# Optimization experiments

Hardware: AMD Instinct MI355X
Metric: run time of the kernel (lower is better)

The kernel has to match this reference:

```python
import jax, jax.numpy as jnp
import numpy as np
from jax import lax

B, M, N = 4096, 306, 984
LAMBDA = 0.1
MAX_ITER = 50


def setup_inputs() -> dict:
    key = jax.random.key(0)
    k1, k2, k3, k4 = jax.random.split(key, 4)
    return {
        "r_real": jax.random.normal(k1, (B, M), dtype=jnp.float32),
        "r_imag": jax.random.normal(k2, (B, M), dtype=jnp.float32),
        # phi buffer: torch.randn(M, N, dtype=complex64) -> real/imag each ~N(0, 1/2)?
        # torch.randn(complex64) draws real & imag each from N(0, 1/sqrt(2)^2)=N(0,0.5).
        "phi_real": jax.random.normal(k3, (M, N), dtype=jnp.float32) * np.float32(1.0 / np.sqrt(2.0)),
        "phi_imag": jax.random.normal(k4, (M, N), dtype=jnp.float32) * np.float32(1.0 / np.sqrt(2.0)),
    }


def reference(r_real, r_imag, phi_real, phi_imag):
    phi = (phi_real + 1j * phi_imag).astype(jnp.complex64)          # [M, N]
    r = (r_real + 1j * r_imag).astype(jnp.complex64)                # [B, M]
    # step_size = 1 / ||phi||_2^2  (spectral norm squared)
    step = (1.0 / jnp.linalg.norm(phi, ord=2) ** 2).real.astype(jnp.float32)
    thresh = (LAMBDA * step).astype(jnp.float32)
    phi_c = jnp.conj(phi)

    def body(w, _):
        # error = w @ phi.T - r : [B, M]
        error = jnp.einsum("bn,mn->bm", w, phi) - r
        # gradient = error @ conj(phi) : [B, N]
        grad = jnp.einsum("bm,mn->bn", error, phi_c)
        w_next = w - step * grad
        w_mag = jnp.abs(w_next)
        new_mag = jax.nn.relu(w_mag - thresh)
        # polar(new_mag, angle(w_next))
        w_new = (new_mag * jnp.exp(1j * jnp.angle(w_next))).astype(jnp.complex64)
        return w_new, None

    w0 = jnp.zeros((r.shape[0], N), dtype=jnp.complex64)
    w, _ = lax.scan(body, w0, None, length=MAX_ITER)
    return jnp.abs(w).astype(jnp.float32)
```

## Files before the change

kernel.cpp:

```cpp
#include <hip/hip_runtime.h>
#include <math.h>

#define Bb 4096
#define Mm 306
#define Nn 984
#define NCP 1024
#define KA 2048
#define ITERS 50
#define KSQ 9

typedef _Float16 f16x8 __attribute__((ext_vector_type(8)));
typedef float f32x16 __attribute__((ext_vector_type(16)));

__device__ __forceinline__ void cmac(float2& c, const float2 a, const float2 b) {
    c.x = fmaf(a.x, b.x, c.x);
    c.x = fmaf(-a.y, b.y, c.x);
    c.y = fmaf(a.x, b.y, c.y);
    c.y = fmaf(a.y, b.x, c.y);
}

__device__ __forceinline__ unsigned short f16bits(float v) {
    union { _Float16 h; unsigned short u; } cv;
    cv.h = (_Float16)v;
    return cv.u;
}
__device__ __forceinline__ float f16lo(unsigned int u) {
    union { unsigned short s; _Float16 h; } cv; cv.s = (unsigned short)(u & 0xffffu);
    return (float)cv.h;
}
__device__ __forceinline__ float f16hi(unsigned int u) {
    union { unsigned short s; _Float16 h; } cv; cv.s = (unsigned short)(u >> 16);
    return (float)cv.h;
}

__device__ __forceinline__ void load_lds16(const void* g, void* l) {
    __builtin_amdgcn_global_load_lds((const __attribute__((address_space(1))) void*)g,
                                     (__attribute__((address_space(3))) void*)l, 16, 0, 0);
}

__device__ __forceinline__ size_t swzA(int b, int c) {
    return ((size_t)(((b >> 7) * 32 + (c >> 5)) * 1024 + ((c >> 2) & 7) * 128 + (b & 127))) * 4 + (c & 3);
}
__device__ __forceinline__ size_t swzB(int jr, int q) {
    return ((size_t)(((jr >> 7) * 32 + (q >> 5)) * 1024 + ((q >> 2) & 7) * 128 + (jr & 127))) * 4 + (q & 3);
}
__device__ __forceinline__ size_t swzA2(int b, int c) {
    return ((size_t)(((b >> 7) * 10 + (c >> 5)) * 1024 + ((c >> 2) & 7) * 128 + (b & 127))) * 4 + (c & 3);
}
__device__ __forceinline__ size_t swzB2(int jr, int q) {
    return ((size_t)(((jr >> 7) * 10 + (q >> 5)) * 1024 + ((q >> 2) & 7) * 128 + (jr & 127))) * 4 + (q & 3);
}

__global__ void gram_kernel(const float* __restrict__ pr, const float* __restrict__ pi,
                            float2* __restrict__ G) {
    __shared__ float2 As[32][33];
    __shared__ float2 Bs[32][33];
    int tx = threadIdx.x, ty = threadIdx.y;
    int t = ty * 16 + tx;
    int i0 = blockIdx.y * 32, j0 = blockIdx.x * 32;
    int zs = blockIdx.z * 246;
    int ze = zs + 246 < Nn ? zs + 246 : Nn;
    float2 acc[2][2] = {};
    for (int k0 = zs; k0 < ze; k0 += 32) {
        #pragma unroll
        for (int rep = 0; rep < 4; ++rep) {
            int idx = t + rep * 256;
            int rr = idx >> 5, cc = idx & 31;
            int gk = k0 + cc;
            int gi = i0 + rr, gj = j0 + rr;
            float2 a = make_float2(0.f, 0.f), b = make_float2(0.f, 0.f);
            if (gk < ze) {
                if (gi < Mm) a = make_float2(pr[(size_t)gi * Nn + gk], pi[(size_t)gi * Nn + gk]);
                if (gj < Mm) b = make_float2(pr[(size_t)gj * Nn + gk], pi[(size_t)gj * Nn + gk]);
            }
            As[rr][cc] = a; Bs[rr][cc] = b;
        }
        __syncthreads();
        #pragma unroll 8
        for (int kk = 0; kk < 32; ++kk) {
            float2 a0 = As[ty * 2][kk], a1 = As[ty * 2 + 1][kk];
            float2 b0 = Bs[tx * 2][kk], b1 = Bs[tx * 2 + 1][kk];
            #define GMAC(qq, aa, bb) \
                qq.x = fmaf(aa.x, bb.x, qq.x); qq.x = fmaf(aa.y, bb.y, qq.x); \
                qq.y = fmaf(aa.y, bb.x, qq.y); qq.y = fmaf(-aa.x, bb.y, qq.y);
            GMAC(acc[0][0], a0, b0) GMAC(acc[0][1], a0, b1)
            GMAC(acc[1][0], a1, b0) GMAC(acc[1][1], a1, b1)
            #undef GMAC
        }
        __syncthreads();
    }
    #pragma unroll
    for (int i = 0; i < 2; ++i) {
        int gi = i0 + ty * 2 + i;
        #pragma unroll
        for (int j = 0; j < 2; ++j) {
            int gj = j0 + tx * 2 + j;
            if (gi < Mm && gj < Mm) {
                atomicAdd(&G[gi * Mm + gj].x, acc[i][j].x);
                atomicAdd(&G[gi * Mm + gj].y, acc[i][j].y);
            }
        }
    }
}

__global__ void frobz_kernel(const float2* __restrict__ H, float* __restrict__ slot,
                             float2* __restrict__ dst, int n) {
    int idx = blockIdx.x * blockDim.x + threadIdx.x;
    int stride = gridDim.x * blockDim.x;
    float s = 0.f;
    for (int i = idx; i < n; i += stride) {
        float2 v = H[i];
        s = fmaf(v.x, v.x, s);
        s = fmaf(v.y, v.y, s);
        dst[i] = make_float2(0.f, 0.f);
    }
    #pragma unroll
    for (int o = 32; o > 0; o >>= 1) s += __shfl_down(s, o, 64);
    __shared__ float wsum[4];
    int lane = threadIdx.x & 63, wv = threadIdx.x >> 6;
    if (lane == 0) wsum[wv] = s;
    __syncthreads();
    if (threadIdx.x == 0) atomicAdd(slot, wsum[0] + wsum[1] + wsum[2] + wsum[3]);
}

__global__ void sqmm_kernel(const float2* __restrict__ A, float2* __restrict__ C,
                            const float* __restrict__ fslot) {
    __shared__ float2 As[32][33];
    __shared__ float2 Bs[32][33];
    float inv = 1.0f / fslot[0];
    int tx = threadIdx.x, ty = threadIdx.y;
    int t = ty * 16 + tx;
    int r0 = blockIdx.y * 32, c0 = blockIdx.x * 32;
    int zs = blockIdx.z * 80;
    int ze = zs + 80 < Mm ? zs + 80 : Mm;
    float2 acc[2][2] = {};
    for (int k0 = zs; k0 < ze; k0 += 32) {
        #pragma unroll
        for (int i = 0; i < 4; ++i) {
            int idx = t + i * 256;
            int rr = idx >> 5, cc = idx & 31;
            int gr = r0 + rr, gk = k0 + cc;
            As[rr][cc] = (gr < Mm && gk < ze) ? A[gr * Mm + gk] : make_float2(0.f, 0.f);
            int gk2 = k0 + rr, gc = c0 + cc;
            Bs[rr][cc] = (gk2 < ze && gc < Mm) ? A[gk2 * Mm + gc] : make_float2(0.f, 0.f);
        }
        __syncthreads();
        #pragma unroll 8
        for (int kk = 0; kk < 32; ++kk) {
            float2 a0 = As[ty * 2][kk], a1 = As[ty * 2 + 1][kk];
            float2 b0 = Bs[kk][tx * 2], b1 = Bs[kk][tx * 2 + 1];
            cmac(acc[0][0], a0, b0); cmac(acc[0][1], a0, b1);
            cmac(acc[1][0], a1, b0); cmac(acc[1][1], a1, b1);
        }
        __syncthreads();
    }
    #pragma unroll
    for (int i = 0; i < 2; ++i) {
        int gr = r0 + ty * 2 + i;
        #pragma unroll
        for (int j = 0; j < 2; ++j) {
            int gc = c0 + tx * 2 + j;
            if (gr < Mm && gc < Mm) {
                atomicAdd(&C[gr * Mm + gc].x, acc[i][j].x * inv);
                atomicAdd(&C[gr * Mm + gc].y, acc[i][j].y * inv);
            }
        }
    }
}

__global__ void ray1_kernel(const float2* __restrict__ H, float2* __restrict__ v) {
    int t = blockIdx.x;
    int k = threadIdx.x;
    float sx = 0.f, sy = 0.f;
    for (int j = k; j < Mm; j += 256) {
        float2 h = H[(size_t)t * Mm + j];
        sx += h.x; sy += h.y;
    }
    #pragma unroll
    for (int o = 32; o > 0; o >>= 1) { sx += __shfl_down(sx, o, 64); sy += __shfl_down(sy, o, 64); }
    __shared__ float wx[4], wy[4];
    int lane = k & 63, wv = k >> 6;
    if (lane == 0) { wx[wv] = sx; wy[wv] = sy; }
    __syncthreads();
    if (k == 0) v[t] = make_float2(wx[0] + wx[1] + wx[2] + wx[3],
                                   wy[0] + wy[1] + wy[2] + wy[3]);
}

__global__ void ray2_kernel(const float2* __restrict__ G, const float2* __restrict__ v,
                            float* __restrict__ slots) {
    int t = blockIdx.x;
    int k0 = threadIdx.x;
    float ux = 0.f, uy = 0.f;
    for (int k = k0; k < Mm; k += 256) {
        float2 g = G[(size_t)k * Mm + t];
        float2 vk = v[k];
        ux = fmaf(g.x, vk.x, ux); ux = fmaf(g.y, vk.y, ux);
        uy = fmaf(g.x, vk.y, uy); uy = fmaf(-g.y, vk.x, uy);
    }
    #pragma unroll
    for (int o = 32; o > 0; o >>= 1) { ux += __shfl_down(ux, o, 64); uy += __shfl_down(uy, o, 64); }
    __shared__ float wx[4], wy[4];
    int lane = k0 & 63, wv = k0 >> 6;
    if (lane == 0) { wx[wv] = ux; wy[wv] = uy; }
    __syncthreads();
    if (k0 == 0) {
        float sux = wx[0] + wx[1] + wx[2] + wx[3];
        float suy = wy[0] + wy[1] + wy[2] + wy[3];
        float2 vt = v[t];
        atomicAdd(&slots[16], vt.x * sux + vt.y * suy);
        atomicAdd(&slots[17], vt.x * vt.x + vt.y * vt.y);
    }
}

__global__ void ray3_kernel(const float* __restrict__ slots, float* __restrict__ sc) {
    float step = slots[17] / slots[16];
    sc[0] = step;
    sc[1] = 0.1f * step;
}

__global__ void qpack_kernel(const float* __restrict__ pr, const float* __restrict__ pi,
                             unsigned int* __restrict__ Bu, const float* __restrict__ sc) {
    __shared__ float2 Pn[16][33];
    __shared__ float2 Pc[16][65];
    float nstep = -sc[0];
    int t = threadIdx.x;
    int tx = t & 15, ty = t >> 4;
    int n0 = blockIdx.x * 32, c0 = blockIdx.y * 64;
    float2 q[2][4] = {};
    for (int m0 = 0; m0 < Mm; m0 += 16) {
        #pragma unroll
        for (int rep = 0; rep < 6; ++rep) {
            int idx = t + rep * 256;
            if (idx < 512) {
                int mm = idx >> 5, col = idx & 31;
                int gm = m0 + mm;
                float2 a = make_float2(0.f, 0.f);
                if (gm < Mm && n0 + col < Nn)
                    a = make_float2(pr[(size_t)gm * Nn + n0 + col], pi[(size_t)gm * Nn + n0 + col]);
                Pn[mm][col] = a;
            } else {
                int idx2 = idx - 512;
                int mm = idx2 >> 6, col = idx2 & 63;
                int gm = m0 + mm;
                float2 b = make_float2(0.f, 0.f);
                if (gm < Mm && c0 + col < Nn)
                    b = make_float2(pr[(size_t)gm * Nn + c0 + col], pi[(size_t)gm * Nn + c0 + col]);
                Pc[mm][col] = b;
            }
        }
        __syncthreads();
        #pragma unroll
        for (int mm = 0; mm < 16; ++mm) {
            float2 a0 = Pn[mm][ty * 2], a1 = Pn[mm][ty * 2 + 1];
            float2 b0 = Pc[mm][tx * 4], b1 = Pc[mm][tx * 4 + 1];
            float2 b2 = Pc[mm][tx * 4 + 2], b3 = Pc[mm][tx * 4 + 3];
            #define QMAC(qq, aa, bb) \
                qq.x = fmaf(aa.x, bb.x, qq.x); qq.x = fmaf(aa.y, bb.y, qq.x); \
                qq.y = fmaf(aa.y, bb.x, qq.y); qq.y = fmaf(-aa.x, bb.y, qq.y);
            QMAC(q[0][0], a0, b0) QMAC(q[0][1], a0, b1) QMAC(q[0][2], a0, b2) QMAC(q[0][3], a0, b3)
            QMAC(q[1][0], a1, b0) QMAC(q[1][1], a1, b1) QMAC(q[1][2], a1, b2) QMAC(q[1][3], a1, b3)
            #undef QMAC
        }
        __syncthreads();
    }
    #pragma unroll
    for (int i = 0; i < 2; ++i) {
        int n = n0 + ty * 2 + i;
        #pragma unroll
        for (int j = 0; j < 4; ++j) {
            int c = c0 + tx * 4 + j;
            if (n < Nn && c < Nn) {
                float MR = fmaf(nstep, q[i][j].x, (n == c) ? 1.0f : 0.0f);
                float MI = nstep * q[i][j].y;
                unsigned short hR = f16bits(MR);
                unsigned short hI = f16bits(MI);
                unsigned short nhI = hI ^ 0x8000u;
                int jr = ((c >> 5) * 64) + (c & 31);
                Bu[swzB(jr, n)]      = (unsigned)hR | ((unsigned)nhI << 16);
                Bu[swzB(jr + 32, n)] = (unsigned)hI | ((unsigned)hR << 16);
            }
        }
    }
}

__global__ void rpack_kernel(const float* __restrict__ rr, const float* __restrict__ ri,
                             unsigned int* __restrict__ rp16) {
    int b = blockIdx.x * 256 + threadIdx.x;
    int m = blockIdx.y;
    rp16[swzA2(b, m)] = (unsigned)f16bits(rr[(size_t)b * Mm + m]) |
                        ((unsigned)f16bits(ri[(size_t)b * Mm + m]) << 16);
}

__global__ void ppack2_kernel(const float* __restrict__ pr, const float* __restrict__ pi,
                              unsigned int* __restrict__ B2u, const float* __restrict__ sc) {
    int n = blockIdx.x * 256 + threadIdx.x;
    int m = blockIdx.y;
    if (n >= Nn) return;
    float s = sc[0];
    float xr = pr[(size_t)m * Nn + n], xi = pi[(size_t)m * Nn + n];
    unsigned short x = f16bits(-s * xr), y = f16bits(-s * xi);
    int jr2 = ((n >> 5) * 64) + (n & 31);
    B2u[swzB2(jr2, m)]      = (unsigned)x | ((unsigned)y << 16);
    B2u[swzB2(jr2 + 32, m)] = (unsigned)(y ^ 0x8000u) | ((unsigned)x << 16);
}

__global__ __launch_bounds__(256, 2) void rphi_mfma_kernel(
    const _Float16* __restrict__ rp16, const _Float16* __restrict__ B2,
    unsigned int* __restrict__ rph16) {
    __shared__ _Float16 As[8192];
    __shared__ _Float16 Bs[8192];
    int tid = threadIdx.x;
    int lane = tid & 63, wv = tid >> 6;
    int wm = wv & 1, wn = wv >> 1;
    int bblk = blockIdx.x, nblk = blockIdx.y;
    int l31 = lane & 31, lh = lane >> 5;

    f32x16 acc[2][2] = {};

    for (int kt = 0; kt < 10; ++kt) {
        #pragma unroll
        for (int c = 0; c < 4; ++c) {
            int u = c * 256 + tid;
            const char* ga = (const char*)rp16 + (((size_t)(bblk * 10 + kt)) * 1024 + u) * 16;
            load_lds16(ga, &As[(size_t)(c * 256 + wv * 64) * 8]);
            const char* gb = (const char*)B2 + (((size_t)(nblk * 10 + kt)) * 1024 + u) * 16;
            load_lds16(gb, &Bs[(size_t)(c * 256 + wv * 64) * 8]);
        }
        __syncthreads();
        #pragma unroll
        for (int s = 0; s < 4; ++s) {
            int kq = s * 2 + lh;
            f16x8 af[2], bfr[2];
            #pragma unroll
            for (int mt = 0; mt < 2; ++mt)
                af[mt] = *reinterpret_cast<const f16x8*>(
                    &As[(size_t)(kq * 128 + wm * 64 + mt * 32 + l31) * 8]);
            #pragma unroll
            for (int nt = 0; nt < 2; ++nt)
                bfr[nt] = *reinterpret_cast<const f16x8*>(
                    &Bs[(size_t)(kq * 128 + wn * 64 + nt * 32 + l31) * 8]);
            #pragma unroll
            for (int mt = 0; mt < 2; ++mt)
                #pragma unroll
                for (int nt = 0; nt < 2; ++nt)
                    acc[mt][nt] = __builtin_amdgcn_mfma_f32_32x32x16_f16(af[mt], bfr[nt], acc[mt][nt], 0, 0, 0);
        }
        __syncthreads();
    }

    int b0 = bblk * 128;
    int c = nblk * 64 + wn * 32 + l31;
    #pragma unroll
    for (int mt = 0; mt < 2; ++mt) {
        #pragma unroll
        for (int reg = 0; reg < 16; ++reg) {
            int row = b0 + wm * 64 + mt * 32 + ((reg & 3) + 8 * (reg >> 2) + 4 * lh);
            rph16[(size_t)row * NCP + c] =
                (unsigned)f16bits(-acc[mt][0][reg]) | ((unsigned)f16bits(-acc[mt][1][reg]) << 16);
        }
    }
}

__global__ __launch_bounds__(512) void ista9_kernel(
    const _Float16* __restrict__ wfi, const _Float16* __restrict__ Bq,
    unsigned int* __restrict__ wfo,
    const unsigned int* __restrict__ rph16,
    const float* __restrict__ sc, float* __restrict__ out, int last) {
    __shared__ _Float16 As0[8192], As1[8192];
    __shared__ _Float16 Bs0[2][8192], Bs1[2][8192];
    int tid = threadIdx.x;
    int lane = tid & 63, wv = tid >> 6;
    int wm = wv >> 2, wn = wv & 3;
    int id = blockIdx.x;
    int x = id & 7;
    int n = id >> 3;
    int bblk = (x & 3) * 8 + (n & 7);
    int nb2  = (x >> 2) * 4 + (n >> 3);
    int l31 = lane & 31, lh = lane >> 5;
    int slab = wn >> 1, chg = wn & 1;

    f32x16 acc[2][2] = {};

    const char* gA  = (const char*)wfi + (size_t)bblk * 32 * 1024 * 16;
    const char* gB0 = (const char*)Bq + (size_t)(nb2 * 2 + 0) * 32 * 1024 * 16;
    const char* gB1 = (const char*)Bq + (size_t)(nb2 * 2 + 1) * 32 * 1024 * 16;

    #define STAGE9(kt, Ad, Bd)                                                        \
        {                                                                             \
            _Float16* Ap = (Ad);                                                      \
            _Float16* Bp0 = &(Bd)[0][0];                                              \
            _Float16* Bp1 = &(Bd)[1][0];                                              \
            _Pragma("unroll")                                                         \
            for (int cc = 0; cc < 2; ++cc) {                                          \
                int u = cc * 512 + tid;                                               \
                size_t ldst = (size_t)(cc * 512 + wv * 64) * 8;                       \
                load_lds16(gA + ((size_t)(kt) * 1024 + u) * 16, &Ap[ldst]);           \
                load_lds16(gB0 + ((size_t)(kt) * 1024 + u) * 16, &Bp0[ldst]);         \
                load_lds16(gB1 + ((size_t)(kt) * 1024 + u) * 16, &Bp1[ldst]);         \
            }                                                                         \
        }

    #define COMPUTE9(Asrc, Bsrc)                                                      \
        {                                                                             \
            _Pragma("unroll")                                                         \
            for (int s = 0; s < 4; ++s) {                                             \
                int kq = s * 2 + lh;                                                  \
                f16x8 af[2], bf[2];                                                   \
                _Pragma("unroll")                                                     \
                for (int mt = 0; mt < 2; ++mt)                                        \
                    af[mt] = *reinterpret_cast<const f16x8*>(                         \
                        &(Asrc)[(size_t)(kq * 128 + wm * 64 + mt * 32 + l31) * 8]);   \
                _Pragma("unroll")                                                     \
                for (int nt = 0; nt < 2; ++nt)                                        \
                    bf[nt] = *reinterpret_cast<const f16x8*>(                         \
                        &(Bsrc)[slab][(size_t)(kq * 128 + chg * 64 + nt * 32 + l31) * 8]); \
                _Pragma("unroll")                                                     \
                for (int mt = 0; mt < 2; ++mt)                                        \
                    _Pragma("unroll")                                                 \
                    for (int nt = 0; nt < 2; ++nt)                                    \
                        acc[mt][nt] = __builtin_amdgcn_mfma_f32_32x32x16_f16(         \
                            af[mt], bf[nt], acc[mt][nt], 0, 0, 0);                    \
            }                                                                         \
        }

    STAGE9(0, As0, Bs0);
    for (int kt = 0; kt < 32; kt += 2) {
        STAGE9(kt + 1, As1, Bs1);
        asm volatile("s_waitcnt vmcnt(6)" ::: "memory");
        __builtin_amdgcn_s_barrier();
        COMPUTE9(As0, Bs0);
        __builtin_amdgcn_s_barrier();
        STAGE9(kt + 2, As0, Bs0);
        asm volatile("s_waitcnt vmcnt(6)" ::: "memory");
        __builtin_amdgcn_s_barrier();
        COMPUTE9(As1, Bs1);
        __builtin_amdgcn_s_barrier();
    }
    #undef STAGE9
    #undef COMPUTE9

    float thr = sc[1];
    int b0 = bblk * 128;
    int c = nb2 * 128 + wn * 32 + l31;
    #pragma unroll
    for (int mt = 0; mt < 2; ++mt) {
        #pragma unroll
        for (int reg = 0; reg < 16; ++reg) {
            int row = b0 + wm * 64 + mt * 32 + ((reg & 3) + 8 * (reg >> 2) + 4 * lh);
            unsigned int ru = rph16[(size_t)row * NCP + c];
            float zr = acc[mt][0][reg] + f16lo(ru);
            float zi = acc[mt][1][reg] + f16hi(ru);
            float mag = sqrtf(zr * zr + zi * zi);
            float nm = mag - thr;
            float f = (nm > 0.f) ? (nm / mag) : 0.f;
            wfo[swzA(row, c)] = (unsigned)f16bits(zr * f) | ((unsigned)f16bits(zi * f) << 16);
            if (last && c < Nn) out[(size_t)row * Nn + c] = fmaxf(nm, 0.f);
        }
    }
}

extern "C" void kernel_launch(void* const* d_in, const int* in_sizes, int n_in,
                              void* d_out, int out_size, void* d_ws, size_t ws_size,
                              hipStream_t stream) {
    const float* rr = (const float*)d_in[0];
    const float* ri = (const float*)d_in[1];
    const float* pr = (const float*)d_in[2];
    const float* pi = (const float*)d_in[3];
    float* out = (float*)d_out;

    char* ws = (char*)d_ws;
    size_t off = 0;
    _Float16* wf0 = (_Float16*)(ws + off); off += (size_t)Bb * KA * sizeof(_Float16);
    _Float16* wf1 = (_Float16*)(ws + off); off += (size_t)Bb * KA * sizeof(_Float16);
    _Float16* Bq  = (_Float16*)(ws + off); off += (size_t)2048 * 2048 * sizeof(_Float16);
    unsigned int* rph16 = (unsigned int*)(ws + off); off += (size_t)Bb * NCP * 4;
    _Float16* rp16 = (_Float16*)(ws + off); off += (size_t)Bb * 640 * sizeof(_Float16);
    _Float16* B2  = (_Float16*)(ws + off); off += (size_t)2048 * 640 * sizeof(_Float16);
    float2* G = (float2*)(ws + off);     off += (size_t)Mm * Mm * sizeof(float2);
    float2* H1 = (float2*)(ws + off);    off += (size_t)Mm * Mm * sizeof(float2);
    float2* H2 = (float2*)(ws + off);    off += (size_t)Mm * Mm * sizeof(float2);
    float2* vvec = (float2*)(ws + off);  off += (size_t)Mm * sizeof(float2);
    float* slots = (float*)(ws + off);   off += 64 * sizeof(float);
    float* sc = slots + 32;

    (void)hipMemsetAsync(wf0, 0, (size_t)Bb * KA * sizeof(_Float16), stream);
    (void)hipMemsetAsync(Bq, 0, (size_t)2048 * 2048 * sizeof(_Float16), stream);
    (void)hipMemsetAsync(rp16, 0, (size_t)Bb * 640 * sizeof(_Float16), stream);
    (void)hipMemsetAsync(B2, 0, (size_t)2048 * 640 * sizeof(_Float16), stream);
    (void)hipMemsetAsync(slots, 0, 64 * sizeof(float), stream);
    (void)hipMemsetAsync(G, 0, (size_t)Mm * Mm * sizeof(float2), stream);

    gram_kernel<<<dim3(10, 10, 4), dim3(16, 16), 0, stream>>>(pr, pi, G);
    float2* bufs[2] = { H1, H2 };
    const float2* src = G;
    for (int s = 0; s < KSQ; ++s) {
        float2* dst = bufs[s & 1];
        frobz_kernel<<<128, 256, 0, stream>>>(src, slots + s, dst, Mm * Mm);
        sqmm_kernel<<<dim3(10, 10, 4), dim3(16, 16), 0, stream>>>(src, dst, slots + s);
        src = dst;
    }
    ray1_kernel<<<Mm, 256, 0, stream>>>(src, vvec);
    ray2_kernel<<<Mm, 256, 0, stream>>>(G, vvec, slots);
    ray3_kernel<<<1, 1, 0, stream>>>(slots, sc);

    qpack_kernel<<<dim3(31, 16), 256, 0, stream>>>(pr, pi, (unsigned int*)Bq, sc);
    rpack_kernel<<<dim3(16, Mm), 256, 0, stream>>>(rr, ri, (unsigned int*)rp16);
    ppack2_kernel<<<dim3(4, Mm), 256, 0, stream>>>(pr, pi, (unsigned int*)B2, sc);
    rphi_mfma_kernel<<<dim3(32, 16), 256, 0, stream>>>(rp16, B2, rph16);

    _Float16* wbuf[2] = { wf0, wf1 };
    for (int it = 0; it < ITERS; ++it) {
        ista9_kernel<<<256, 512, 0, stream>>>(
            wbuf[it & 1], Bq, (unsigned int*)wbuf[(it + 1) & 1], rph16, sc, out,
            it == ITERS - 1 ? 1 : 0);
    }
}
```

Measured before the change: 2.882 ms.

## Interleave ISTA MFMA phases with split global-to-LDS staging and priority hints

The ISTA iteration kernel's k-tile compute is split into four barrier-separated phases. Part of the next tile's B prefetch is issued inside the first phase, and each MFMA group is wrapped in s_setprio so waves overlap memory issue with matrix math. The vmcnt wait drops from 6 to 4 to match the new load split. The one-time qpack kernel also changes its column mapping to strided per-thread access, meant to reduce LDS bank conflicts. The cost is many more workgroup barriers per tile, which may add stalls.

```diff
diff --git a/kernel.cpp b/kernel.cpp
--- a/kernel.cpp
+++ b/kernel.cpp
@@ -252,8 +252,8 @@
         #pragma unroll
         for (int mm = 0; mm < 16; ++mm) {
             float2 a0 = Pn[mm][ty * 2], a1 = Pn[mm][ty * 2 + 1];
-            float2 b0 = Pc[mm][tx * 4], b1 = Pc[mm][tx * 4 + 1];
-            float2 b2 = Pc[mm][tx * 4 + 2], b3 = Pc[mm][tx * 4 + 3];
+            float2 b0 = Pc[mm][tx], b1 = Pc[mm][16 + tx];
+            float2 b2 = Pc[mm][32 + tx], b3 = Pc[mm][48 + tx];
             #define QMAC(qq, aa, bb) \
                 qq.x = fmaf(aa.x, bb.x, qq.x); qq.x = fmaf(aa.y, bb.y, qq.x); \
                 qq.y = fmaf(aa.y, bb.x, qq.y); qq.y = fmaf(-aa.x, bb.y, qq.y);
@@ -268,7 +268,7 @@
         int n = n0 + ty * 2 + i;
         #pragma unroll
         for (int j = 0; j < 4; ++j) {
-            int c = c0 + tx * 4 + j;
+            int c = c0 + j * 16 + tx;
             if (n < Nn && c < Nn) {
                 float MR = fmaf(nstep, q[i][j].x, (n == c) ? 1.0f : 0.0f);
                 float MI = nstep * q[i][j].y;
@@ -361,7 +361,7 @@
     }
 }
 
-__global__ __launch_bounds__(512) void ista9_kernel(
+__global__ __launch_bounds__(512) void ista10_kernel(
     const _Float16* __restrict__ wfi, const _Float16* __restrict__ Bq,
     unsigned int* __restrict__ wfo,
     const unsigned int* __restrict__ rph16,
@@ -385,59 +385,65 @@
     const char* gB0 = (const char*)Bq + (size_t)(nb2 * 2 + 0) * 32 * 1024 * 16;
     const char* gB1 = (const char*)Bq + (size_t)(nb2 * 2 + 1) * 32 * 1024 * 16;
 
-    #define STAGE9(kt, Ad, Bd)                                                        \
+    #define STAGE_A(kt, Ad, Bd)                                                       \
         {                                                                             \
-            _Float16* Ap = (Ad);                                                      \
-            _Float16* Bp0 = &(Bd)[0][0];                                              \
-            _Float16* Bp1 = &(Bd)[1][0];                                              \
-            _Pragma("unroll")                                                         \
-            for (int cc = 0; cc < 2; ++cc) {                                          \
-                int u = cc * 512 + tid;                                               \
-                size_t ldst = (size_t)(cc * 512 + wv * 64) * 8;                       \
-                load_lds16(gA + ((size_t)(kt) * 1024 + u) * 16, &Ap[ldst]);           \
-                load_lds16(gB0 + ((size_t)(kt) * 1024 + u) * 16, &Bp0[ldst]);         \
-                load_lds16(gB1 + ((size_t)(kt) * 1024 + u) * 16, &Bp1[ldst]);         \
-            }                                                                         \
-        }
-
-    #define COMPUTE9(Asrc, Bsrc)                                                      \
+            size_t ld0 = (size_t)(wv * 64) * 8;                                       \
+            size_t ld1 = (size_t)(512 + wv * 64) * 8;                                 \
+            load_lds16(gA + ((size_t)(kt) * 1024 + tid) * 16, &(Ad)[ld0]);            \
+            load_lds16(gB0 + ((size_t)(kt) * 1024 + tid) * 16, &(Bd)[0][ld0]);        \
+            load_lds16(gB1 + ((size_t)(kt) * 1024 + tid) * 16, &(Bd)[1][ld0]);        \
+            load_lds16(gA + ((size_t)(kt) * 1024 + 512 + tid) * 16, &(Ad)[ld1]);      \
+        }
+    #define STAGE_B(kt, Bd)                                                           \
         {                                                                             \
-            _Pragma("unroll")                                                         \
-            for (int s = 0; s < 4; ++s) {                                             \
-                int kq = s * 2 + lh;                                                  \
-                f16x8 af[2], bf[2];                                                   \
-                _Pragma("unroll")                                                     \
-                for (int mt = 0; mt < 2; ++mt)                                        \
-                    af[mt] = *reinterpret_cast<const f16x8*>(                         \
-                        &(Asrc)[(size_t)(kq * 128 + wm * 64 + mt * 32 + l31) * 8]);   \
-                _Pragma("unroll")                                                     \
-                for (int nt = 0; nt < 2; ++nt)                                        \
-                    bf[nt] = *reinterpret_cast<const f16x8*>(                         \
-                        &(Bsrc)[slab][(size_t)(kq * 128 + chg * 64 + nt * 32 + l31) * 8]); \
-                _Pragma("unroll")                                                     \
-                for (int mt = 0; mt < 2; ++mt)                                        \
-                    _Pragma("unroll")                                                 \
-                    for (int nt = 0; nt < 2; ++nt)                                    \
-                        acc[mt][nt] = __builtin_amdgcn_mfma_f32_32x32x16_f16(         \
-                            af[mt], bf[nt], acc[mt][nt], 0, 0, 0);                    \
-            }                                                                         \
-        }
-
-    STAGE9(0, As0, Bs0);
+            size_t ld1 = (size_t)(512 + wv * 64) * 8;                                 \
+            load_lds16(gB0 + ((size_t)(kt) * 1024 + 512 + tid) * 16, &(Bd)[0][ld1]);  \
+            load_lds16(gB1 + ((size_t)(kt) * 1024 + 512 + tid) * 16, &(Bd)[1][ld1]);  \
+        }
+
+    #define PHASE(Asrc, Bsrc, S, STAGESTMT)                                           \
+        {                                                                             \
+            const int kq_ = (S) * 2 + lh;                                             \
+            f16x8 af0 = *reinterpret_cast<const f16x8*>(                              \
+                &(Asrc)[(size_t)(kq_ * 128 + wm * 64 + l31) * 8]);                    \
+            f16x8 af1 = *reinterpret_cast<const f16x8*>(                              \
+                &(Asrc)[(size_t)(kq_ * 128 + wm * 64 + 32 + l31) * 8]);               \
+            f16x8 bf0 = *reinterpret_cast<const f16x8*>(                              \
+                &(Bsrc)[slab][(size_t)(kq_ * 128 + chg * 64 + l31) * 8]);             \
+            f16x8 bf1 = *reinterpret_cast<const f16x8*>(                              \
+                &(Bsrc)[slab][(size_t)(kq_ * 128 + chg * 64 + 32 + l31) * 8]);        \
+            STAGESTMT;                                                                \
+            __builtin_amdgcn_s_barrier();                                             \
+            __builtin_amdgcn_s_setprio(1);                                            \
+            acc[0][0] = __builtin_amdgcn_mfma_f32_32x32x16_f16(af0, bf0, acc[0][0], 0, 0, 0); \
+            acc[0][1] = __builtin_amdgcn_mfma_f32_32x32x16_f16(af0, bf1, acc[0][1], 0, 0, 0); \
+            acc[1][0] = __builtin_amdgcn_mfma_f32_32x32x16_f16(af1, bf0, acc[1][0], 0, 0, 0); \
+            acc[1][1] = __builtin_amdgcn_mfma_f32_32x32x16_f16(af1, bf1, acc[1][1], 0, 0, 0); \
+            __builtin_amdgcn_s_setprio(0);                                            \
+            __builtin_amdgcn_s_barrier();                                             \
+        }
+
+    STAGE_A(0, As0, Bs0);
+    STAGE_B(0, Bs0);
     for (int kt = 0; kt < 32; kt += 2) {
-        STAGE9(kt + 1, As1, Bs1);
-        asm volatile("s_waitcnt vmcnt(6)" ::: "memory");
+        STAGE_A(kt + 1, As1, Bs1);
+        asm volatile("s_waitcnt vmcnt(4)" ::: "memory");
         __builtin_amdgcn_s_barrier();
-        COMPUTE9(As0, Bs0);
+        PHASE(As0, Bs0, 0, STAGE_B(kt + 1, Bs1));
+        PHASE(As0, Bs0, 1, );
+        PHASE(As0, Bs0, 2, );
+        PHASE(As0, Bs0, 3, );
+        STAGE_A(kt + 2, As0, Bs0);
+        asm volatile("s_waitcnt vmcnt(4)" ::: "memory");
         __builtin_amdgcn_s_barrier();
-        STAGE9(kt + 2, As0, Bs0);
-        asm volatile("s_waitcnt vmcnt(6)" ::: "memory");
-        __builtin_amdgcn_s_barrier();
-        COMPUTE9(As1, Bs1);
-        __builtin_amdgcn_s_barrier();
-    }
-    #undef STAGE9
-    #undef COMPUTE9
+        PHASE(As1, Bs1, 0, STAGE_B(kt + 2, Bs0));
+        PHASE(As1, Bs1, 1, );
+        PHASE(As1, Bs1, 2, );
+        PHASE(As1, Bs1, 3, );
+    }
+    #undef PHASE
+    #undef STAGE_A
+    #undef STAGE_B
 
     float thr = sc[1];
     int b0 = bblk * 128;
@@ -510,7 +516,7 @@
 
     _Float16* wbuf[2] = { wf0, wf1 };
     for (int it = 0; it < ITERS; ++it) {
-        ista9_kernel<<<256, 512, 0, stream>>>(
+        ista10_kernel<<<256, 512, 0, stream>>>(
             wbuf[it & 1], Bq, (unsigned int*)wbuf[(it + 1) & 1], rph16, sc, out,
             it == ITERS - 1 ? 1 : 0);
     }
```

After: 3.018 ms. 4.7% more time.
